# Performance work log

Measured on AMD Instinct MI355X. Metric: run time of the kernel, lower is better.

## Reference

```python
import jax, jax.numpy as jnp
import numpy as np

B, S, D = 2, 2048, 2560
H, HD = 32, 80           # n_head, head_dim = n_embd // n_head
RD = 32                  # rotary_dim (partial rotary, phi-style)
ROPE_BASE = 10000.0


def _rope_cache(seqlen, rotary_dim):
    # inv_freq = 1 / base^(2i/d); freqs = outer(t, inv_freq)  -> [S, RD//2]
    inv_freq = 1.0 / (ROPE_BASE ** (jnp.arange(0, rotary_dim, 2, dtype=jnp.float32) / rotary_dim))
    t = jnp.arange(seqlen, dtype=jnp.float32)
    freqs = jnp.outer(t, inv_freq)
    return jnp.cos(freqs), jnp.sin(freqs)


def setup_inputs() -> dict:
    key = jax.random.key(0)
    k0, k1, k2, k3, k4 = jax.random.split(key, 5)
    x = jax.random.normal(k0, (B, S, D), dtype=jnp.float32)
    wqkv_w = jax.random.normal(k1, (3 * D, D), dtype=jnp.float32) * 0.02
    wqkv_b = jax.random.normal(k2, (3 * D,), dtype=jnp.float32) * 0.02
    out_w = jax.random.normal(k3, (D, D), dtype=jnp.float32) * 0.02
    out_b = jax.random.normal(k4, (D,), dtype=jnp.float32) * 0.02
    return {"x": x, "wqkv_w": wqkv_w, "wqkv_b": wqkv_b, "out_w": out_w, "out_b": out_b}


def _attention_core(x, wqkv_w, wqkv_b, out_w, out_b):
    b, s, d = x.shape
    qkv = (x @ wqkv_w.T + wqkv_b).reshape(b, s, 3, H, HD)  # [B,S,3,H,HD]

    cos, sin = _rope_cache(s, RD)            # [S, RD//2]
    c = cos[:, None, :]                       # [S,1,RD//2]
    si = sin[:, None, :]

    def rot(t):  # partial NeoX-style rotary on first RD dims; t: [B,S,H,HD]
        t_rot, t_pass = t[..., :RD], t[..., RD:]
        t1, t2 = t_rot[..., : RD // 2], t_rot[..., RD // 2 :]
        return jnp.concatenate([t1 * c - t2 * si, t1 * si + t2 * c, t_pass], axis=-1)

    q = rot(qkv[:, :, 0])                     # [B,S,H,HD]
    k = rot(qkv[:, :, 1])
    v = qkv[:, :, 2]

    # fp32 scores = q @ (k * scale)^T, causal mask filled with -10000.0 (as in source)
    scale = 1.0 / np.sqrt(HD).astype(np.float32)
    scores = jnp.einsum("bqhd,bkhd->bhqk", q, k * scale)  # [B,H,S,S]
    causal_mask = jnp.arange(s)[None, :] > jnp.arange(s)[:, None]  # cols > rows
    scores = jnp.where(causal_mask, jnp.float32(-10000.0), scores)
    attn = jax.nn.softmax(scores, axis=-1)
    ctx = jnp.einsum("bhqk,bkhd->bqhd", attn, v).reshape(b, s, d)
    return ctx @ out_w.T + out_b


def reference(x, wqkv_w, wqkv_b, out_w, out_b):
    return _attention_core(x, wqkv_w, wqkv_b, out_w, out_b)
```

## Files before the change

kernel.cpp:

```cpp
#include <hip/hip_runtime.h>
#include <cstdint>
#include <cstddef>

#define B_  2
#define S_  2048
#define D_  2560
#define H_  32
#define HD_ 80

typedef __attribute__((ext_vector_type(8))) short  short8;
typedef __attribute__((ext_vector_type(4))) float  floatx4;

__device__ __forceinline__ float b2f(unsigned short u) {
  union { unsigned int i; float f; } x; x.i = ((unsigned int)u) << 16; return x.f;
}
__device__ __forceinline__ unsigned short f2bf(float f) {
  union { float f; unsigned int i; } x; x.f = f;
  unsigned int u = x.i;
  return (unsigned short)((u + 0x7fffu + ((u >> 16) & 1u)) >> 16);
}

__global__ void cvt3_kernel(const float* __restrict__ s0, unsigned short* __restrict__ d0, int n0,
                            const float* __restrict__ s1, unsigned short* __restrict__ d1, int n1,
                            const float* __restrict__ s2, unsigned short* __restrict__ d2, int n2) {
  int j = blockIdx.x * 256 + threadIdx.x;
  const float* s; unsigned short* d;
  if (j < n0) { s = s0; d = d0; }
  else {
    j -= n0;
    if (j < n1) { s = s1; d = d1; }
    else { j -= n1; if (j >= n2) return; s = s2; d = d2; }
  }
  const float4 v = ((const float4*)s)[j];
  ushort4 r;
  r.x = f2bf(v.x); r.y = f2bf(v.y); r.z = f2bf(v.z); r.w = f2bf(v.w);
  ((ushort4*)d)[j] = r;
}

#define GLOAD_LDS16(g, l)                                                      \
  __builtin_amdgcn_global_load_lds(                                            \
      (const __attribute__((address_space(1))) void*)(g),                      \
      (__attribute__((address_space(3))) void*)(l), 16, 0, 0)

template <int OUT_BF16, int MSUB>
__global__ __launch_bounds__(512)
void gemm256(const unsigned short* __restrict__ A,
             const unsigned short* __restrict__ Bw,
             const float* __restrict__ bias,
             void* __restrict__ Cv,
             const int M, const int N, const int K) {
  constexpr int ASH  = MSUB * 2048;
  constexpr int BSH  = 16384;
  constexpr int CBUF = ASH + BSH;
  __shared__ __align__(16) unsigned short sh[2 * CBUF];
  const int tid  = threadIdx.x;
  const int wave = tid >> 6;
  const int lane = tid & 63;
  const int wm = wave >> 2;
  const int wn = wave & 3;
  const int fr = lane & 15;
  const int fg = lane >> 4;
  const int row0 = (int)blockIdx.y * (MSUB * 32);
  const int col0 = (int)blockIdx.x << 8;
  const unsigned short* Ab = A  + (size_t)row0 * K;
  const unsigned short* Bb = Bw + (size_t)col0 * K;
  const int srow = lane >> 2;
  const int scol = ((lane & 3) << 3) ^ ((lane & 32) ? 16 : 0);
  const int rdoff = fr * 32 + ((fg * 8) ^ ((fr & 8) ? 16 : 0));
  const int aOff = wm * (MSUB == 8 ? 8192 : 2048);
  const int bOff = ASH + (wn >> 1) * 8192;
  const int rbB  = (wn & 1) * 4;
  const int NT = K >> 6;

  floatx4 acc[MSUB][4] = {};

#define STAGE_HALF(G, matOff, c, h, k0)                                        \
  do {                                                                         \
    _Pragma("unroll")                                                          \
    for (int i_ = 0; i_ < 2; ++i_) {                                           \
      const int s_ = (wave << 1) | i_;                                         \
      const int kk_ = s_ >> 3, rb_ = s_ & 7;                                   \
      GLOAD_LDS16((G) + (size_t)((h) * 128 + rb_ * 16 + srow) * K              \
                      + ((k0) + kk_ * 32 + scol),                              \
                  &sh[(c) * CBUF + (matOff) + (h) * 8192 + s_ * 512]);         \
    }                                                                          \
  } while (0)

  STAGE_HALF(Ab, 0, 0, 0, 0);
  if (MSUB == 8) STAGE_HALF(Ab, 0, 0, 1, 0);
  STAGE_HALF(Bb, ASH, 0, 0, 0);
  STAGE_HALF(Bb, ASH, 0, 1, 0);
  asm volatile("s_waitcnt vmcnt(0)" ::: "memory");
  __builtin_amdgcn_s_barrier();

  for (int t = 0; t < NT; ++t) {
    const int c  = t & 1;
    const int cb = c * CBUF;
    if (t + 1 < NT) {
      const int k1 = (t + 1) << 6;
      STAGE_HALF(Ab, 0, c ^ 1, 0, k1);
      if (MSUB == 8) STAGE_HALF(Ab, 0, c ^ 1, 1, k1);
      STAGE_HALF(Bb, ASH, c ^ 1, 0, k1);
      STAGE_HALF(Bb, ASH, c ^ 1, 1, k1);
    }
    short8 aL[4][2], aH[4][2], bF0[2][2], bF1[2][2];
#pragma unroll
    for (int nj = 0; nj < 2; ++nj)
#pragma unroll
      for (int kk = 0; kk < 2; ++kk)
        bF0[nj][kk] = *(const short8*)&sh[cb + bOff + (kk * 8 + rbB + nj) * 512 + rdoff];
#pragma unroll
    for (int mi = 0; mi < 4; ++mi)
#pragma unroll
      for (int kk = 0; kk < 2; ++kk)
        aL[mi][kk] = *(const short8*)&sh[cb + aOff + (kk * 8 + mi) * 512 + rdoff];
#pragma unroll
    for (int nj = 0; nj < 2; ++nj)
#pragma unroll
      for (int kk = 0; kk < 2; ++kk)
        bF1[nj][kk] = *(const short8*)&sh[cb + bOff + (kk * 8 + rbB + 2 + nj) * 512 + rdoff];
    __builtin_amdgcn_s_setprio(1);
#pragma unroll
    for (int kk = 0; kk < 2; ++kk)
#pragma unroll
      for (int mi = 0; mi < 4; ++mi)
#pragma unroll
        for (int nj = 0; nj < 2; ++nj)
          acc[mi][nj] = __builtin_amdgcn_mfma_f32_16x16x32_bf16(aL[mi][kk], bF0[nj][kk], acc[mi][nj], 0, 0, 0);
    __builtin_amdgcn_s_setprio(0);
    if (MSUB == 8) {
#pragma unroll
      for (int mi = 0; mi < 4; ++mi)
#pragma unroll
        for (int kk = 0; kk < 2; ++kk)
          aH[mi][kk] = *(const short8*)&sh[cb + aOff + (kk * 8 + 4 + mi) * 512 + rdoff];
    }
    __builtin_amdgcn_s_setprio(1);
#pragma unroll
    for (int kk = 0; kk < 2; ++kk)
#pragma unroll
      for (int mi = 0; mi < 4; ++mi)
#pragma unroll
        for (int nj = 0; nj < 2; ++nj)
          acc[mi][2 + nj] = __builtin_amdgcn_mfma_f32_16x16x32_bf16(aL[mi][kk], bF1[nj][kk], acc[mi][2 + nj], 0, 0, 0);
    if (MSUB == 8) {
#pragma unroll
      for (int kk = 0; kk < 2; ++kk)
#pragma unroll
        for (int mi = 0; mi < 4; ++mi)
#pragma unroll
          for (int nj = 0; nj < 2; ++nj)
            acc[4 + mi][2 + nj] = __builtin_amdgcn_mfma_f32_16x16x32_bf16(aH[mi][kk], bF1[nj][kk], acc[4 + mi][2 + nj], 0, 0, 0);
#pragma unroll
      for (int kk = 0; kk < 2; ++kk)
#pragma unroll
        for (int mi = 0; mi < 4; ++mi)
#pragma unroll
          for (int nj = 0; nj < 2; ++nj)
            acc[4 + mi][nj] = __builtin_amdgcn_mfma_f32_16x16x32_bf16(aH[mi][kk], bF0[nj][kk], acc[4 + mi][nj], 0, 0, 0);
    }
    __builtin_amdgcn_s_setprio(0);
    if (t + 1 < NT) {
      asm volatile("s_waitcnt vmcnt(0)" ::: "memory");
      __builtin_amdgcn_s_barrier();
    }
  }
#undef STAGE_HALF

  unsigned short* Cb = (unsigned short*)Cv;
  float* Cf = (float*)Cv;
#pragma unroll
  for (int nj = 0; nj < 4; ++nj) {
    const int col = col0 + wn * 64 + nj * 16 + fr;
    const float bv = bias[col];
#pragma unroll
    for (int mi = 0; mi < MSUB; ++mi) {
      const int rowb = row0 + wm * (MSUB * 16) + mi * 16 + fg * 4;
#pragma unroll
      for (int r = 0; r < 4; ++r) {
        const float v = acc[mi][nj][r] + bv;
        const size_t idx = (size_t)(rowb + r) * N + col;
        if (OUT_BF16) Cb[idx] = f2bf(v);
        else          Cf[idx] = v;
      }
    }
  }
}

__global__ void rope_kernel(const unsigned short* __restrict__ qkv,
                            unsigned short* __restrict__ Q,
                            unsigned short* __restrict__ K) {
  const int idx = blockIdx.x * 256 + threadIdx.x;
  if (idx >= B_ * S_ * H_) return;
  const int h = idx & (H_ - 1);
  const int s = (idx >> 5) & (S_ - 1);
  const int b = idx >> 16;
  const unsigned short* row = qkv + (size_t)(b * S_ + s) * (3 * D_);
  const size_t obase = ((size_t)(b * H_ + h) * S_ + s) * HD_;

  float cc[16], ssn[16];
#pragma unroll
  for (int i = 0; i < 16; i++) {
    const float ang = (float)s * exp2f((float)i * -0.83048202372184059f);
    ssn[i] = sinf(ang);
    cc[i]  = cosf(ang);
  }
  {
    const float QS = 0.11180339887498949f * 1.4426950408889634f;
    const uint4* src = (const uint4*)(row + h * HD_);
    float f[80], g[80];
#pragma unroll
    for (int i = 0; i < 10; i++) {
      uint4 t = src[i];
      const unsigned short* w = (const unsigned short*)&t;
#pragma unroll
      for (int j = 0; j < 8; j++) f[i * 8 + j] = b2f(w[j]);
    }
#pragma unroll
    for (int i = 0; i < 16; i++) {
      g[i]      = f[i] * cc[i] - f[i + 16] * ssn[i];
      g[i + 16] = f[i] * ssn[i] + f[i + 16] * cc[i];
    }
#pragma unroll
    for (int i = 32; i < 80; i++) g[i] = f[i];
    uint4* dst = (uint4*)(Q + obase);
#pragma unroll
    for (int i = 0; i < 10; i++) {
      uint4 t;
      unsigned short* w = (unsigned short*)&t;
#pragma unroll
      for (int j = 0; j < 8; j++) w[j] = f2bf(g[i * 8 + j] * QS);
      dst[i] = t;
    }
  }
  {
    const uint4* src = (const uint4*)(row + (H_ + h) * HD_);
    float f[32], g[32];
#pragma unroll
    for (int i = 0; i < 4; i++) {
      uint4 t = src[i];
      const unsigned short* w = (const unsigned short*)&t;
#pragma unroll
      for (int j = 0; j < 8; j++) f[i * 8 + j] = b2f(w[j]);
    }
#pragma unroll
    for (int i = 0; i < 16; i++) {
      g[i]      = f[i] * cc[i] - f[i + 16] * ssn[i];
      g[i + 16] = f[i] * ssn[i] + f[i + 16] * cc[i];
    }
    uint4* dst = (uint4*)(K + obase);
#pragma unroll
    for (int i = 0; i < 4; i++) {
      uint4 t;
      unsigned short* w = (unsigned short*)&t;
#pragma unroll
      for (int j = 0; j < 8; j++) w[j] = f2bf(g[i * 8 + j]);
      dst[i] = t;
    }
#pragma unroll
    for (int i = 4; i < 10; i++) dst[i] = src[i];
  }
}

__global__ __launch_bounds__(256)
void vtrans_kernel(const unsigned short* __restrict__ qkv, unsigned short* __restrict__ Vt) {
  __shared__ unsigned short T[64][88];
  const int tid = threadIdx.x;
  const int bh = blockIdx.y;
  const int b = bh >> 5, h = bh & 31;
  const int tile = blockIdx.x;
  const int s0 = tile * 64;
  for (int t = tid; t < 640; t += 256) {
    const int r = t / 10, c = t % 10;
    const size_t src = ((size_t)((b * S_ + s0 + r) * 3) + 2) * D_ + h * HD_ + c * 8;
    *(uint4*)&T[r][c * 8] = *(const uint4*)&qkv[src];
  }
  __syncthreads();
  unsigned short* tb = Vt + ((size_t)bh * 32 + tile) * 5120;
  for (int t = tid; t < 640; t += 256) {
    const int d = t / 8, sc = t % 8;
    uint4 o;
    unsigned short* w = (unsigned short*)&o;
#pragma unroll
    for (int j = 0; j < 8; j++) w[j] = T[sc * 8 + j][d];
    *(uint4*)&tb[d * 64 + ((sc * 8) ^ ((d & 7) * 8))] = o;
  }
}

__global__ __launch_bounds__(256, 4)
void attn_mfma(const unsigned short* __restrict__ Qg,
               const unsigned short* __restrict__ Kg,
               const unsigned short* __restrict__ Vtg,
               unsigned short* __restrict__ ctx) {
  __shared__ unsigned short Ks[64 * 80];
  __shared__ unsigned short Vs[80 * 64];
  __shared__ unsigned short Ts[4][32 * 40];

  const int tid  = threadIdx.x;
  const int wave = tid >> 6;
  const int lane = tid & 63;
  const int fr   = lane & 15;
  const int fg   = lane >> 4;
  const int bh   = blockIdx.y;
  const int qt   = (int)gridDim.x - 1 - (int)blockIdx.x;
  const int qbase = (qt << 7) + wave * 32;

  const unsigned short* Qrow  = Qg  + (size_t)bh * S_ * HD_;
  const unsigned short* Krow  = Kg  + (size_t)bh * S_ * HD_;
  const unsigned short* Vtile = Vtg + (size_t)bh * 32 * 5120;

  short8 qf[2][3];
  const short8 zfrag = {};
#pragma unroll
  for (int mi = 0; mi < 2; mi++) {
    const unsigned short* qp = Qrow + (size_t)(qbase + mi * 16 + fr) * HD_;
    qf[mi][0] = *(const short8*)&qp[fg * 8];
    qf[mi][1] = *(const short8*)&qp[32 + fg * 8];
    qf[mi][2] = (fg < 2) ? *(const short8*)&qp[64 + fg * 8] : zfrag;
  }

  floatx4 accOT[5][2] = {};
  float l_part[2] = {0.f, 0.f};

  const int nch = 2 * qt + 2;
  for (int c = 0; c < nch; c++) {
    const int k0 = c * 64;
    __syncthreads();
    {
      const unsigned short* Kt = Krow + (size_t)k0 * HD_;
      for (int i = wave; i < 10; i += 4)
        GLOAD_LDS16(Kt + i * 512 + lane * 8, &Ks[i * 512]);
    }
    {
      const unsigned short* Vt = Vtile + (size_t)c * 5120;
      for (int i = wave; i < 10; i += 4)
        GLOAD_LDS16(Vt + i * 512 + lane * 8, &Vs[i * 512]);
    }
    __syncthreads();

    floatx4 accST[4][2] = {};
#pragma unroll
    for (int ni = 0; ni < 4; ni++) {
      const unsigned short* kp = &Ks[(ni * 16 + fr) * 80];
      const short8 kf0 = *(const short8*)&kp[fg * 8];
      const short8 kf1 = *(const short8*)&kp[32 + fg * 8];
      const short8 kf2 = *(const short8*)&kp[64 + (fg & 1) * 8];
      accST[ni][0] = __builtin_amdgcn_mfma_f32_16x16x32_bf16(kf0, qf[0][0], accST[ni][0], 0, 0, 0);
      accST[ni][1] = __builtin_amdgcn_mfma_f32_16x16x32_bf16(kf0, qf[1][0], accST[ni][1], 0, 0, 0);
      accST[ni][0] = __builtin_amdgcn_mfma_f32_16x16x32_bf16(kf1, qf[0][1], accST[ni][0], 0, 0, 0);
      accST[ni][1] = __builtin_amdgcn_mfma_f32_16x16x32_bf16(kf1, qf[1][1], accST[ni][1], 0, 0, 0);
      accST[ni][0] = __builtin_amdgcn_mfma_f32_16x16x32_bf16(kf2, qf[0][2], accST[ni][0], 0, 0, 0);
      accST[ni][1] = __builtin_amdgcn_mfma_f32_16x16x32_bf16(kf2, qf[1][2], accST[ni][1], 0, 0, 0);
    }

    if (k0 + 63 > qbase) {
#pragma unroll
      for (int ni = 0; ni < 4; ni++)
#pragma unroll
        for (int mi = 0; mi < 2; mi++) {
          const int qg = qbase + mi * 16 + fr;
#pragma unroll
          for (int r = 0; r < 4; r++) {
            const int kg = k0 + ni * 16 + fg * 4 + r;
            if (kg > qg) accST[ni][mi][r] = -1e30f;
          }
        }
    }

#pragma unroll
    for (int hh = 0; hh < 2; hh++) {
#pragma unroll
      for (int nh = 0; nh < 2; nh++) {
        const int ni = hh * 2 + nh;
#pragma unroll
        for (int mi = 0; mi < 2; mi++) {
          const float p0 = __builtin_amdgcn_exp2f(accST[ni][mi][0]);
          const float p1 = __builtin_amdgcn_exp2f(accST[ni][mi][1]);
          const float p2 = __builtin_amdgcn_exp2f(accST[ni][mi][2]);
          const float p3 = __builtin_amdgcn_exp2f(accST[ni][mi][3]);
          l_part[mi] += (p0 + p1) + (p2 + p3);
          uint2 w;
          w.x = (unsigned)f2bf(p0) | ((unsigned)f2bf(p1) << 16);
          w.y = (unsigned)f2bf(p2) | ((unsigned)f2bf(p3) << 16);
          *(uint2*)&Ts[wave][(mi * 16 + fr) * 40 + nh * 16 + fg * 4] = w;
        }
      }
      const short8 pf0 = *(const short8*)&Ts[wave][fr * 40 + fg * 8];
      const short8 pf1 = *(const short8*)&Ts[wave][(16 + fr) * 40 + fg * 8];
      const int vcol = hh * 32 + fg * 8;
#pragma unroll
      for (int dt = 0; dt < 5; dt++) {
        const short8 vf = *(const short8*)&Vs[(dt * 16 + fr) * 64 + (vcol ^ ((fr & 7) * 8))];
        accOT[dt][0] = __builtin_amdgcn_mfma_f32_16x16x32_bf16(vf, pf0, accOT[dt][0], 0, 0, 0);
        accOT[dt][1] = __builtin_amdgcn_mfma_f32_16x16x32_bf16(vf, pf1, accOT[dt][1], 0, 0, 0);
      }
    }
  }

  const int b = bh >> 5, h2 = bh & 31;
#pragma unroll
  for (int mi = 0; mi < 2; mi++) {
    float s = l_part[mi];
    s += __shfl_xor(s, 16);
    s += __shfl_xor(s, 32);
    const float inv = 1.f / s;
    const size_t rowoff = (size_t)(b * S_ + qbase + mi * 16 + fr) * D_ + h2 * HD_;
#pragma unroll
    for (int dt = 0; dt < 5; dt++) {
      const float v0 = accOT[dt][mi][0] * inv;
      const float v1 = accOT[dt][mi][1] * inv;
      const float v2 = accOT[dt][mi][2] * inv;
      const float v3 = accOT[dt][mi][3] * inv;
      uint2 w;
      w.x = (unsigned)f2bf(v0) | ((unsigned)f2bf(v1) << 16);
      w.y = (unsigned)f2bf(v2) | ((unsigned)f2bf(v3) << 16);
      *(uint2*)&ctx[rowoff + dt * 16 + fg * 4] = w;
    }
  }
}

extern "C" void kernel_launch(void* const* d_in, const int* in_sizes, int n_in,
                              void* d_out, int out_size, void* d_ws, size_t ws_size,
                              hipStream_t stream) {
  (void)in_sizes; (void)n_in; (void)out_size; (void)ws_size;
  const float* x      = (const float*)d_in[0];
  const float* wqkv_w = (const float*)d_in[1];
  const float* wqkv_b = (const float*)d_in[2];
  const float* out_w  = (const float*)d_in[3];
  const float* out_b  = (const float*)d_in[4];
  char* ws = (char*)d_ws;

  unsigned short* Xb    = (unsigned short*)(ws + 0);
  unsigned short* Wqkvb = (unsigned short*)(ws + 20971520);
  unsigned short* qkv   = (unsigned short*)(ws + 60293120);
  unsigned short* Qb    = (unsigned short*)(ws + 123207680);
  unsigned short* Kb    = (unsigned short*)(ws + 144179200);
  unsigned short* Woutb = (unsigned short*)(ws + 165150720);
  unsigned short* ctx   = Xb;
  unsigned short* Vtile = (unsigned short*)(ws + 34078720);

  cvt3_kernel<<<35840, 256, 0, stream>>>(x, Xb, 2621440,
                                         wqkv_w, Wqkvb, 4915200,
                                         out_w, Woutb, 1638400);
  gemm256<1, 8><<<dim3(30, 16), 512, 0, stream>>>(Xb, Wqkvb, wqkv_b, (void*)qkv, 4096, 7680, 2560);
  rope_kernel<<<512, 256, 0, stream>>>(qkv, Qb, Kb);
  vtrans_kernel<<<dim3(32, 64), 256, 0, stream>>>(qkv, Vtile);
  attn_mfma<<<dim3(16, 64), 256, 0, stream>>>(Qb, Kb, Vtile, ctx);
  gemm256<0, 4><<<dim3(10, 32), 512, 0, stream>>>(ctx, Woutb, out_b, d_out, 4096, 2560, 2560);
}
```

Before: 603.0 us.

## Double-buffer attention K/V staging, remap blocks across XCDs, enlarge out-proj tile

After: 544.5 us. -9.7%, faster.

```diff
diff --git a/kernel.cpp b/kernel.cpp
--- a/kernel.cpp
+++ b/kernel.cpp
@@ -60,8 +60,14 @@
   const int wn = wave & 3;
   const int fr = lane & 15;
   const int fg = lane >> 4;
-  const int row0 = (int)blockIdx.y * (MSUB * 32);
-  const int col0 = (int)blockIdx.x << 8;
+  int fid = (int)(blockIdx.y * gridDim.x + blockIdx.x);
+  const int nwg = (int)(gridDim.x * gridDim.y);
+  const int cpx = nwg >> 3;
+  fid = (fid & 7) * cpx + (fid >> 3);
+  const int bx = fid % (int)gridDim.x;
+  const int by = fid / (int)gridDim.x;
+  const int row0 = by * (MSUB * 32);
+  const int col0 = bx << 8;
   const unsigned short* Ab = A  + (size_t)row0 * K;
   const unsigned short* Bb = Bw + (size_t)col0 * K;
   const int srow = lane >> 2;
@@ -287,13 +293,13 @@
   }
 }
 
-__global__ __launch_bounds__(256, 4)
+__global__ __launch_bounds__(256, 3)
 void attn_mfma(const unsigned short* __restrict__ Qg,
                const unsigned short* __restrict__ Kg,
                const unsigned short* __restrict__ Vtg,
                unsigned short* __restrict__ ctx) {
-  __shared__ unsigned short Ks[64 * 80];
-  __shared__ unsigned short Vs[80 * 64];
+  __shared__ unsigned short Ks[2][64 * 80];
+  __shared__ unsigned short Vs[2][80 * 64];
   __shared__ unsigned short Ts[4][32 * 40];
 
   const int tid  = threadIdx.x;
@@ -301,8 +307,10 @@
   const int lane = tid & 63;
   const int fr   = lane & 15;
   const int fg   = lane >> 4;
-  const int bh   = blockIdx.y;
-  const int qt   = (int)gridDim.x - 1 - (int)blockIdx.x;
+  int p = (int)(blockIdx.y * gridDim.x + blockIdx.x);
+  p = (p & 7) * 128 + (p >> 3);
+  const int bh = p >> 4;
+  const int qt = 15 - (p & 15);
   const int qbase = (qt << 7) + wave * 32;
 
   const unsigned short* Qrow  = Qg  + (size_t)bh * S_ * HD_;
@@ -323,25 +331,34 @@
   float l_part[2] = {0.f, 0.f};
 
   const int nch = 2 * qt + 2;
+
+#define STAGE_CHUNK(c)                                                         \
+  do {                                                                         \
+    const int buf_ = (c) & 1;                                                  \
+    const unsigned short* Kt_ = Krow + (size_t)(c) * 64 * HD_;                 \
+    const unsigned short* Vt_ = Vtile + (size_t)(c) * 5120;                    \
+    _Pragma("unroll")                                                          \
+    for (int u_ = 0; u_ < 5; ++u_) {                                           \
+      const int j_ = wave * 5 + u_;                                            \
+      if (j_ < 10) GLOAD_LDS16(Kt_ + j_ * 512 + lane * 8, &Ks[buf_][j_ * 512]);\
+      else GLOAD_LDS16(Vt_ + (j_ - 10) * 512 + lane * 8,                       \
+                       &Vs[buf_][(j_ - 10) * 512]);                            \
+    }                                                                          \
+  } while (0)
+
+  STAGE_CHUNK(0);
+
   for (int c = 0; c < nch; c++) {
     const int k0 = c * 64;
-    __syncthreads();
-    {
-      const unsigned short* Kt = Krow + (size_t)k0 * HD_;
-      for (int i = wave; i < 10; i += 4)
-        GLOAD_LDS16(Kt + i * 512 + lane * 8, &Ks[i * 512]);
-    }
-    {
-      const unsigned short* Vt = Vtile + (size_t)c * 5120;
-      for (int i = wave; i < 10; i += 4)
-        GLOAD_LDS16(Vt + i * 512 + lane * 8, &Vs[i * 512]);
-    }
-    __syncthreads();
+    const int buf = c & 1;
+    asm volatile("s_waitcnt vmcnt(0)" ::: "memory");
+    __builtin_amdgcn_s_barrier();
+    if (c + 1 < nch) STAGE_CHUNK(c + 1);
 
     floatx4 accST[4][2] = {};
 #pragma unroll
     for (int ni = 0; ni < 4; ni++) {
-      const unsigned short* kp = &Ks[(ni * 16 + fr) * 80];
+      const unsigned short* kp = &Ks[buf][(ni * 16 + fr) * 80];
       const short8 kf0 = *(const short8*)&kp[fg * 8];
       const short8 kf1 = *(const short8*)&kp[32 + fg * 8];
       const short8 kf2 = *(const short8*)&kp[64 + (fg & 1) * 8];
@@ -390,12 +407,13 @@
       const int vcol = hh * 32 + fg * 8;
 #pragma unroll
       for (int dt = 0; dt < 5; dt++) {
-        const short8 vf = *(const short8*)&Vs[(dt * 16 + fr) * 64 + (vcol ^ ((fr & 7) * 8))];
+        const short8 vf = *(const short8*)&Vs[buf][(dt * 16 + fr) * 64 + (vcol ^ ((fr & 7) * 8))];
         accOT[dt][0] = __builtin_amdgcn_mfma_f32_16x16x32_bf16(vf, pf0, accOT[dt][0], 0, 0, 0);
         accOT[dt][1] = __builtin_amdgcn_mfma_f32_16x16x32_bf16(vf, pf1, accOT[dt][1], 0, 0, 0);
       }
     }
   }
+#undef STAGE_CHUNK
 
   const int b = bh >> 5, h2 = bh & 31;
 #pragma unroll
@@ -446,5 +464,5 @@
   rope_kernel<<<512, 256, 0, stream>>>(qkv, Qb, Kb);
   vtrans_kernel<<<dim3(32, 64), 256, 0, stream>>>(qkv, Vtile);
   attn_mfma<<<dim3(16, 64), 256, 0, stream>>>(Qb, Kb, Vtile, ctx);
-  gemm256<0, 4><<<dim3(10, 32), 512, 0, stream>>>(ctx, Woutb, out_b, d_out, 4096, 2560, 2560);
-}
+  gemm256<0, 8><<<dim3(10, 16), 512, 0, stream>>>(ctx, Woutb, out_b, d_out, 4096, 2560, 2560);
+}
```
